# Performance work log

Hardware: AMD Instinct MI355X
Metric: run time of the kernel (lower is better)

Reference implementation:

```python
import jax, jax.numpy as jnp
import numpy as np

B, S, H, R = 32, 512, 1024, 64


def _bernoulli(key, shape, p=0.05):
    return (jax.random.uniform(key, shape) < p).astype(jnp.float32)


def setup_inputs() -> dict:
    key = jax.random.key(0)
    ks = jax.random.split(key, 16)
    context = jax.random.normal(ks[0], (B, S, H), dtype=jnp.float32)
    masks = jnp.ones((B, S), dtype=jnp.float32)
    all_subject_heads = _bernoulli(ks[1], (B, S))
    all_subject_tails = _bernoulli(ks[2], (B, S))
    # one-hot subject head/tail positions (tail >= head)
    h_pos = jax.random.randint(ks[3], (B,), 0, S // 2)
    t_pos = h_pos + jax.random.randint(ks[4], (B,), 0, 8)
    subject_head = jax.nn.one_hot(h_pos, S, dtype=jnp.float32)
    subject_tail = jax.nn.one_hot(t_pos, S, dtype=jnp.float32)
    object_heads = _bernoulli(ks[5], (B, S, R))
    object_tails = _bernoulli(ks[6], (B, S, R))
    # learned parameters (PyTorch Linear: y = x @ W.T + b; store as [in, out])
    sc = 1.0 / np.sqrt(H)
    Ws_h = jax.random.uniform(ks[7], (H, 1), minval=-sc, maxval=sc)
    bs_h = jnp.zeros((1,), dtype=jnp.float32)
    Ws_t = jax.random.uniform(ks[8], (H, 1), minval=-sc, maxval=sc)
    bs_t = jnp.zeros((1,), dtype=jnp.float32)
    Wo_h = jax.random.uniform(ks[9], (H, R), minval=-sc, maxval=sc)
    bo_h = jnp.zeros((R,), dtype=jnp.float32)
    Wo_t = jax.random.uniform(ks[10], (H, R), minval=-sc, maxval=sc)
    bo_t = jnp.zeros((R,), dtype=jnp.float32)
    return dict(context=context, masks=masks,
                all_subject_heads=all_subject_heads, all_subject_tails=all_subject_tails,
                subject_head=subject_head, subject_tail=subject_tail,
                object_heads=object_heads, object_tails=object_tails,
                Ws_h=Ws_h, bs_h=bs_h, Ws_t=Ws_t, bs_t=bs_t,
                Wo_h=Wo_h, bo_h=bo_h, Wo_t=Wo_t, bo_t=bo_t)


def _bce_with_logits(logits, targets):
    # numerically stable, matches F.binary_cross_entropy_with_logits(reduction='none')
    return jnp.maximum(logits, 0.0) - logits * targets + jnp.log1p(jnp.exp(-jnp.abs(logits)))


def _masked_loss(gold, pred, mask):
    loss = _bce_with_logits(pred, gold)
    if loss.ndim != mask.ndim:
        mask = mask[..., None]
    return jnp.sum(loss * mask) / jnp.sum(mask)


def reference(context, masks, all_subject_heads, all_subject_tails,
              subject_head, subject_tail, object_heads, object_tails,
              Ws_h, bs_h, Ws_t, bs_t, Wo_h, bo_h, Wo_t, bo_t):
    # subject logits: [B,S]
    pred_subject_heads = (context @ Ws_h + bs_h)[..., 0]
    pred_subject_tails = (context @ Ws_t + bs_t)[..., 0]
    # subject pooling: one-hot [B,S] x context [B,S,H] -> [B,H]
    sub_h = jnp.einsum('bs,bsh->bh', subject_head, context)
    sub_t = jnp.einsum('bs,bsh->bh', subject_tail, context)
    subject = (sub_h + sub_t) * 0.5
    context_subject = context + subject[:, None, :]  # [B,S,H]
    pred_object_heads = context_subject @ Wo_h + bo_h  # [B,S,R]
    pred_object_tails = context_subject @ Wo_t + bo_t  # [B,S,R]
    loss = (_masked_loss(all_subject_heads, pred_subject_heads, masks)
            + _masked_loss(all_subject_tails, pred_subject_tails, masks)
            + _masked_loss(object_heads, pred_object_heads, masks)
            + _masked_loss(object_tails, pred_object_tails, masks))
    return loss
```

## Files before the change

kernel.cpp:

```cpp
#include <hip/hip_runtime.h>
#include <hip/hip_bf16.h>


#define B_  32
#define S_  512
#define H_  1024
#define R_  64
#define M_  (B_ * S_)
#define NPAD 160
#define NVALID 130
#define BK 64
#define BKP 72
#define MT 32

typedef __attribute__((ext_vector_type(4))) float  floatx4;
typedef __attribute__((ext_vector_type(8))) short  short8;
typedef __attribute__((ext_vector_type(4))) unsigned short u16x4;
typedef __attribute__((ext_vector_type(8))) unsigned short u16x8;

__device__ __forceinline__ unsigned short f2bf(float f) {
    unsigned int u = __float_as_uint(f);
    u = (u + 0x7FFFu + ((u >> 16) & 1u)) >> 16;
    return (unsigned short)u;
}
__device__ __forceinline__ float bf2f(unsigned short h) {
    return __uint_as_float(((unsigned int)h) << 16);
}

__global__ void prep_weights(const float* __restrict__ Wo_h,
                             const float* __restrict__ Wo_t,
                             const float* __restrict__ Ws_h,
                             const float* __restrict__ Ws_t,
                             unsigned short* __restrict__ WtG) {
    int n = blockIdx.x;
    int tid = threadIdx.x;
    for (int k = tid; k < H_; k += 256) {
        float v;
        if (n < 64)        v = Wo_h[k * R_ + n];
        else if (n < 128)  v = Wo_t[k * R_ + (n - 64)];
        else if (n == 128) v = Ws_h[k];
        else if (n == 129) v = Ws_t[k];
        else               v = 0.0f;
        WtG[n * H_ + k] = f2bf(v);
    }
}

__global__ __launch_bounds__(256) void subj_kernel(
        const float* __restrict__ ctx, const float* __restrict__ head,
        const float* __restrict__ tail, const float* __restrict__ masks,
        const float* __restrict__ Wo_h, const float* __restrict__ Wo_t,
        const float* __restrict__ bo_h, const float* __restrict__ bo_t,
        const float* __restrict__ bs_h, const float* __restrict__ bs_t,
        float* __restrict__ rowBias, float* __restrict__ accum) {
    int b = blockIdx.x, tid = threadIdx.x;
    __shared__ float subj[H_];
    __shared__ int cnt;
    __shared__ int   sidx[8];
    __shared__ float sw[8];
    if (tid == 0) cnt = 0;
    __syncthreads();
    float msk = 0.0f;
    for (int s = tid; s < S_; s += 256) {
        float w = 0.5f * (head[b * S_ + s] + tail[b * S_ + s]);
        if (w != 0.0f) {
            int i = atomicAdd(&cnt, 1);
            if (i < 8) { sidx[i] = s; sw[i] = w; }
        }
        msk += masks[b * S_ + s];
    }
    for (int o = 32; o > 0; o >>= 1) msk += __shfl_down(msk, o, 64);
    if ((tid & 63) == 0) atomicAdd(&accum[1], msk);
    __syncthreads();
    int nnz = cnt < 8 ? cnt : 8;
    for (int h = tid; h < H_; h += 256) {
        float a = 0.0f;
        for (int i = 0; i < nnz; i++)
            a += sw[i] * ctx[((size_t)b * S_ + sidx[i]) * H_ + h];
        subj[h] = a;
    }
    __syncthreads();
    if (tid < NPAD) {
        float bias = tid < 64  ? bo_h[tid]
                   : tid < 128 ? bo_t[tid - 64]
                   : tid == 128 ? bs_h[0]
                   : tid == 129 ? bs_t[0] : 0.0f;
        float acc2 = 0.0f;
        if (tid < 128) {
            const float* W = (tid < 64) ? Wo_h : Wo_t;
            int c = tid & 63;
            for (int k = 0; k < H_; k++) acc2 += subj[k] * W[k * R_ + c];
        }
        rowBias[b * NPAD + tid] = bias + acc2;
    }
}

__global__ __launch_bounds__(256, 2) void main_kernel(
        const float* __restrict__ ctx, const unsigned short* __restrict__ WtG,
        const float* __restrict__ rowBias, const float* __restrict__ masks,
        const float* __restrict__ ash, const float* __restrict__ ast,
        const float* __restrict__ oh, const float* __restrict__ ot,
        float* __restrict__ accum) {
    __shared__ __align__(16) unsigned short Asm[MT * BKP];
    __shared__ __align__(16) unsigned short Bsm[NPAD * BKP];
    __shared__ float rbuf[4];

    const int tid = threadIdx.x;
    const int bm = blockIdx.x;
    const int gm0 = bm * MT;
    const int b = gm0 >> 9;
    const int wave = tid >> 6, lane = tid & 63;
    const int wm = wave & 1;
    const int wn = wave >> 1;
    const int lr = lane & 15, q = lane >> 4;

    const int ar = tid >> 4, af = tid & 15;
    const int bn = tid >> 3, bf = tid & 7;
    const float* aSrc0 = ctx + (size_t)(gm0 + ar) * H_ + af * 4;
    const unsigned short* bSrc0 = WtG + bn * H_ + bf * 8;
    unsigned short* aDst0 = &Asm[ar * BKP + af * 4];
    unsigned short* bDst0 = &Bsm[bn * BKP + bf * 8];

    const int aOff = (wm * 16 + lr) * BKP + q * 8;
    const int bOffBase = (wn * 80 + lr) * BKP + q * 8;

    floatx4 acc[5];
#pragma unroll
    for (int t = 0; t < 5; t++) acc[t] = (floatx4){0.f, 0.f, 0.f, 0.f};

    for (int k0 = 0; k0 < H_; k0 += BK) {
        __syncthreads();
#pragma unroll
        for (int ii = 0; ii < 2; ii++) {
            const float4 v = *(const float4*)(aSrc0 + ii * 16 * H_ + k0);
            u16x4 u = { f2bf(v.x), f2bf(v.y), f2bf(v.z), f2bf(v.w) };
            *(u16x4*)(aDst0 + ii * 16 * BKP) = u;
        }
#pragma unroll
        for (int ii = 0; ii < 5; ii++) {
            u16x8 w = *(const u16x8*)(bSrc0 + ii * 32 * H_ + k0);
            *(u16x8*)(bDst0 + ii * 32 * BKP) = w;
        }
        __syncthreads();
#pragma unroll
        for (int kk = 0; kk < BK; kk += 32) {
            short8 afr = *(const short8*)&Asm[aOff + kk];
#pragma unroll
            for (int t = 0; t < 5; t++) {
                short8 bfr = *(const short8*)&Bsm[bOffBase + t * 16 * BKP + kk];
                acc[t] = __builtin_amdgcn_mfma_f32_16x16x32_bf16(afr, bfr, acc[t], 0, 0, 0);
            }
        }
    }

    float lsum = 0.0f;
#pragma unroll
    for (int t = 0; t < 5; t++) {
        const int col = wn * 80 + t * 16 + lr;
        if (col < NVALID) {
            const float rb = rowBias[b * NPAD + col];
#pragma unroll
            for (int i = 0; i < 4; i++) {
                const int row = gm0 + wm * 16 + q * 4 + i;
                const float l = acc[t][i] + rb;
                float tgt;
                if (col < 64)        tgt = oh[row * R_ + col];
                else if (col < 128)  tgt = ot[row * R_ + (col - 64)];
                else if (col == 128) tgt = ash[row];
                else                 tgt = ast[row];
                const float mk = masks[row];
                const float bce = fmaxf(l, 0.0f) - l * tgt + log1pf(__expf(-fabsf(l)));
                lsum += bce * mk;
            }
        }
    }
    for (int o = 32; o > 0; o >>= 1) lsum += __shfl_down(lsum, o, 64);
    if (lane == 0) rbuf[wave] = lsum;
    __syncthreads();
    if (tid == 0) atomicAdd(&accum[0], rbuf[0] + rbuf[1] + rbuf[2] + rbuf[3]);
}

__global__ void finalize_kernel(const float* __restrict__ accum, float* __restrict__ out) {
    out[0] = accum[0] / accum[1];
}

extern "C" void kernel_launch(void* const* d_in, const int* in_sizes, int n_in,
                              void* d_out, int out_size, void* d_ws, size_t ws_size,
                              hipStream_t stream) {
    const float* ctx   = (const float*)d_in[0];
    const float* masks = (const float*)d_in[1];
    const float* ash   = (const float*)d_in[2];
    const float* ast   = (const float*)d_in[3];
    const float* sh    = (const float*)d_in[4];
    const float* st    = (const float*)d_in[5];
    const float* oh    = (const float*)d_in[6];
    const float* ot    = (const float*)d_in[7];
    const float* Ws_h  = (const float*)d_in[8];
    const float* bs_h  = (const float*)d_in[9];
    const float* Ws_t  = (const float*)d_in[10];
    const float* bs_t  = (const float*)d_in[11];
    const float* Wo_h  = (const float*)d_in[12];
    const float* bo_h  = (const float*)d_in[13];
    const float* Wo_t  = (const float*)d_in[14];
    const float* bo_t  = (const float*)d_in[15];
    float* out = (float*)d_out;

    char* ws = (char*)d_ws;
    float* accum   = (float*)(ws + 0);
    float* rowBias = (float*)(ws + 256);
    unsigned short* WtG = (unsigned short*)(ws + 256 + 32 * NPAD * 4);

    hipMemsetAsync(accum, 0, 8, stream);
    prep_weights<<<NPAD, 256, 0, stream>>>(Wo_h, Wo_t, Ws_h, Ws_t, WtG);
    subj_kernel<<<B_, 256, 0, stream>>>(ctx, sh, st, masks, Wo_h, Wo_t,
                                        bo_h, bo_t, bs_h, bs_t, rowBias, accum);
    main_kernel<<<M_ / MT, 256, 0, stream>>>(ctx, WtG, rowBias, masks,
                                             ash, ast, oh, ot, accum);
    finalize_kernel<<<1, 1, 0, stream>>>(accum, out);
}
```

Before: 167.5 us.

## Load MFMA fragments directly from global with register double-buffering, merge prep kernels

The main GEMM drops LDS staging and its barriers. Each lane now loads its A (fp32, converted to bf16) and B fragments straight from global memory into registers, double-buffered across 32 K-steps. The weight-transpose and subject-bias kernels are merged into one launch, the subject bias matvec is split across two thread halves, and the mask sum moves into the main kernel. In exchange, B fragments are re-read from global/L2 by every wave instead of being shared through LDS, and the subject pooling now caps nonzeros at 4.

```diff
diff --git a/kernel.cpp b/kernel.cpp
--- a/kernel.cpp
+++ b/kernel.cpp
@@ -1,5 +1,4 @@
 #include <hip/hip_runtime.h>
-#include <hip/hip_bf16.h>
 
 
 #define B_  32
@@ -9,69 +8,55 @@
 #define M_  (B_ * S_)
 #define NPAD 160
 #define NVALID 130
-#define BK 64
-#define BKP 72
-#define MT 32
 
 typedef __attribute__((ext_vector_type(4))) float  floatx4;
 typedef __attribute__((ext_vector_type(8))) short  short8;
-typedef __attribute__((ext_vector_type(4))) unsigned short u16x4;
-typedef __attribute__((ext_vector_type(8))) unsigned short u16x8;
 
 __device__ __forceinline__ unsigned short f2bf(float f) {
     unsigned int u = __float_as_uint(f);
     u = (u + 0x7FFFu + ((u >> 16) & 1u)) >> 16;
     return (unsigned short)u;
 }
-__device__ __forceinline__ float bf2f(unsigned short h) {
-    return __uint_as_float(((unsigned int)h) << 16);
-}
-
-__global__ void prep_weights(const float* __restrict__ Wo_h,
-                             const float* __restrict__ Wo_t,
-                             const float* __restrict__ Ws_h,
-                             const float* __restrict__ Ws_t,
-                             unsigned short* __restrict__ WtG) {
-    int n = blockIdx.x;
-    int tid = threadIdx.x;
-    for (int k = tid; k < H_; k += 256) {
-        float v;
-        if (n < 64)        v = Wo_h[k * R_ + n];
-        else if (n < 128)  v = Wo_t[k * R_ + (n - 64)];
-        else if (n == 128) v = Ws_h[k];
-        else if (n == 129) v = Ws_t[k];
-        else               v = 0.0f;
-        WtG[n * H_ + k] = f2bf(v);
-    }
-}
-
-__global__ __launch_bounds__(256) void subj_kernel(
-        const float* __restrict__ ctx, const float* __restrict__ head,
-        const float* __restrict__ tail, const float* __restrict__ masks,
+
+__global__ __launch_bounds__(256) void prep_kernel(
+        const float* __restrict__ ctx,  const float* __restrict__ head,
+        const float* __restrict__ tail,
+        const float* __restrict__ Ws_h, const float* __restrict__ Ws_t,
         const float* __restrict__ Wo_h, const float* __restrict__ Wo_t,
         const float* __restrict__ bo_h, const float* __restrict__ bo_t,
         const float* __restrict__ bs_h, const float* __restrict__ bs_t,
-        float* __restrict__ rowBias, float* __restrict__ accum) {
-    int b = blockIdx.x, tid = threadIdx.x;
+        unsigned short* __restrict__ WtG, float* __restrict__ rowBias) {
+    const int blk = blockIdx.x, tid = threadIdx.x;
+    if (blk < NPAD) {
+        const int n = blk;
+        for (int k = tid; k < H_; k += 256) {
+            float v;
+            if (n < 64)        v = Wo_h[k * R_ + n];
+            else if (n < 128)  v = Wo_t[k * R_ + (n - 64)];
+            else if (n == 128) v = Ws_h[k];
+            else if (n == 129) v = Ws_t[k];
+            else               v = 0.0f;
+            WtG[n * H_ + k] = f2bf(v);
+        }
+        return;
+    }
+    const int b = blk - NPAD;
     __shared__ float subj[H_];
+    __shared__ float part[256];
     __shared__ int cnt;
-    __shared__ int   sidx[8];
-    __shared__ float sw[8];
+    __shared__ int   sidx[4];
+    __shared__ float sw[4];
     if (tid == 0) cnt = 0;
     __syncthreads();
-    float msk = 0.0f;
     for (int s = tid; s < S_; s += 256) {
         float w = 0.5f * (head[b * S_ + s] + tail[b * S_ + s]);
         if (w != 0.0f) {
             int i = atomicAdd(&cnt, 1);
-            if (i < 8) { sidx[i] = s; sw[i] = w; }
-        }
-        msk += masks[b * S_ + s];
-    }
-    for (int o = 32; o > 0; o >>= 1) msk += __shfl_down(msk, o, 64);
-    if ((tid & 63) == 0) atomicAdd(&accum[1], msk);
-    __syncthreads();
-    int nnz = cnt < 8 ? cnt : 8;
+            if (i < 4) { sidx[i] = s; sw[i] = w; }
+        }
+    }
+    __syncthreads();
+    const int nnz = cnt < 4 ? cnt : 4;
     for (int h = tid; h < H_; h += 256) {
         float a = 0.0f;
         for (int i = 0; i < nnz; i++)
@@ -79,77 +64,85 @@
         subj[h] = a;
     }
     __syncthreads();
+    {
+        const int c = tid & 127, hf = tid >> 7;
+        const float* W = (c < 64) ? (Wo_h + c) : (Wo_t + (c - 64));
+        float a = 0.0f;
+        const int k0 = hf * 512;
+#pragma unroll 8
+        for (int k = k0; k < k0 + 512; k++)
+            a += subj[k] * W[(size_t)k * R_];
+        part[tid] = a;
+    }
+    __syncthreads();
     if (tid < NPAD) {
-        float bias = tid < 64  ? bo_h[tid]
-                   : tid < 128 ? bo_t[tid - 64]
-                   : tid == 128 ? bs_h[0]
-                   : tid == 129 ? bs_t[0] : 0.0f;
-        float acc2 = 0.0f;
-        if (tid < 128) {
-            const float* W = (tid < 64) ? Wo_h : Wo_t;
-            int c = tid & 63;
-            for (int k = 0; k < H_; k++) acc2 += subj[k] * W[k * R_ + c];
-        }
-        rowBias[b * NPAD + tid] = bias + acc2;
-    }
-}
-
-__global__ __launch_bounds__(256, 2) void main_kernel(
+        float v;
+        if (tid < 128)
+            v = part[tid] + part[128 + tid] + (tid < 64 ? bo_h[tid] : bo_t[tid - 64]);
+        else if (tid == 128) v = bs_h[0];
+        else if (tid == 129) v = bs_t[0];
+        else                 v = 0.0f;
+        rowBias[b * NPAD + tid] = v;
+    }
+}
+
+__global__ __launch_bounds__(256) void main_kernel(
         const float* __restrict__ ctx, const unsigned short* __restrict__ WtG,
         const float* __restrict__ rowBias, const float* __restrict__ masks,
         const float* __restrict__ ash, const float* __restrict__ ast,
         const float* __restrict__ oh, const float* __restrict__ ot,
         float* __restrict__ accum) {
-    __shared__ __align__(16) unsigned short Asm[MT * BKP];
-    __shared__ __align__(16) unsigned short Bsm[NPAD * BKP];
     __shared__ float rbuf[4];
-
-    const int tid = threadIdx.x;
-    const int bm = blockIdx.x;
-    const int gm0 = bm * MT;
-    const int b = gm0 >> 9;
+    const int tid  = threadIdx.x;
+    const int gm0  = blockIdx.x * 32;
+    const int b    = gm0 >> 9;
     const int wave = tid >> 6, lane = tid & 63;
     const int wm = wave & 1;
     const int wn = wave >> 1;
     const int lr = lane & 15, q = lane >> 4;
 
-    const int ar = tid >> 4, af = tid & 15;
-    const int bn = tid >> 3, bf = tid & 7;
-    const float* aSrc0 = ctx + (size_t)(gm0 + ar) * H_ + af * 4;
-    const unsigned short* bSrc0 = WtG + bn * H_ + bf * 8;
-    unsigned short* aDst0 = &Asm[ar * BKP + af * 4];
-    unsigned short* bDst0 = &Bsm[bn * BKP + bf * 8];
-
-    const int aOff = (wm * 16 + lr) * BKP + q * 8;
-    const int bOffBase = (wn * 80 + lr) * BKP + q * 8;
+    if (tid < 32) {
+        float mv = masks[gm0 + tid];
+#pragma unroll
+        for (int o = 16; o > 0; o >>= 1) mv += __shfl_down(mv, o, 64);
+        if (tid == 0) atomicAdd(&accum[1], mv);
+    }
+
+    const float* aP = ctx + (size_t)(gm0 + wm * 16 + lr) * H_ + q * 8;
+    const unsigned short* bB[5];
+#pragma unroll
+    for (int t = 0; t < 5; t++)
+        bB[t] = WtG + (size_t)(wn * 80 + t * 16 + lr) * H_ + q * 8;
 
     floatx4 acc[5];
 #pragma unroll
     for (int t = 0; t < 5; t++) acc[t] = (floatx4){0.f, 0.f, 0.f, 0.f};
 
-    for (int k0 = 0; k0 < H_; k0 += BK) {
-        __syncthreads();
-#pragma unroll
-        for (int ii = 0; ii < 2; ii++) {
-            const float4 v = *(const float4*)(aSrc0 + ii * 16 * H_ + k0);
-            u16x4 u = { f2bf(v.x), f2bf(v.y), f2bf(v.z), f2bf(v.w) };
-            *(u16x4*)(aDst0 + ii * 16 * BKP) = u;
-        }
-#pragma unroll
-        for (int ii = 0; ii < 5; ii++) {
-            u16x8 w = *(const u16x8*)(bSrc0 + ii * 32 * H_ + k0);
-            *(u16x8*)(bDst0 + ii * 32 * BKP) = w;
-        }
-        __syncthreads();
-#pragma unroll
-        for (int kk = 0; kk < BK; kk += 32) {
-            short8 afr = *(const short8*)&Asm[aOff + kk];
-#pragma unroll
-            for (int t = 0; t < 5; t++) {
-                short8 bfr = *(const short8*)&Bsm[bOffBase + t * 16 * BKP + kk];
-                acc[t] = __builtin_amdgcn_mfma_f32_16x16x32_bf16(afr, bfr, acc[t], 0, 0, 0);
-            }
-        }
+    float4 a0[2], a1[2];
+    short8 bv[2][5];
+    a0[0] = *(const float4*)(aP + 0);
+    a1[0] = *(const float4*)(aP + 4);
+#pragma unroll
+    for (int t = 0; t < 5; t++) bv[0][t] = *(const short8*)(bB[t] + 0);
+
+#pragma unroll
+    for (int i = 0; i < 32; i++) {
+        const int cur = i & 1, nxt = cur ^ 1;
+        if (i < 31) {
+            const int k = (i + 1) * 32;
+            a0[nxt] = *(const float4*)(aP + k);
+            a1[nxt] = *(const float4*)(aP + k + 4);
+#pragma unroll
+            for (int t = 0; t < 5; t++) bv[nxt][t] = *(const short8*)(bB[t] + k);
+        }
+        short8 af;
+        af[0] = (short)f2bf(a0[cur].x); af[1] = (short)f2bf(a0[cur].y);
+        af[2] = (short)f2bf(a0[cur].z); af[3] = (short)f2bf(a0[cur].w);
+        af[4] = (short)f2bf(a1[cur].x); af[5] = (short)f2bf(a1[cur].y);
+        af[6] = (short)f2bf(a1[cur].z); af[7] = (short)f2bf(a1[cur].w);
+#pragma unroll
+        for (int t = 0; t < 5; t++)
+            acc[t] = __builtin_amdgcn_mfma_f32_16x16x32_bf16(af, bv[cur][t], acc[t], 0, 0, 0);
     }
 
     float lsum = 0.0f;
@@ -173,6 +166,7 @@
             }
         }
     }
+#pragma unroll
     for (int o = 32; o > 0; o >>= 1) lsum += __shfl_down(lsum, o, 64);
     if (lane == 0) rbuf[wave] = lsum;
     __syncthreads();
@@ -195,8 +189,8 @@
     const float* oh    = (const float*)d_in[6];
     const float* ot    = (const float*)d_in[7];
     const float* Ws_h  = (const float*)d_in[8];
+    const float* Ws_t  = (const float*)d_in[10];
     const float* bs_h  = (const float*)d_in[9];
-    const float* Ws_t  = (const float*)d_in[10];
     const float* bs_t  = (const float*)d_in[11];
     const float* Wo_h  = (const float*)d_in[12];
     const float* bo_h  = (const float*)d_in[13];
@@ -210,10 +204,10 @@
     unsigned short* WtG = (unsigned short*)(ws + 256 + 32 * NPAD * 4);
 
     hipMemsetAsync(accum, 0, 8, stream);
-    prep_weights<<<NPAD, 256, 0, stream>>>(Wo_h, Wo_t, Ws_h, Ws_t, WtG);
-    subj_kernel<<<B_, 256, 0, stream>>>(ctx, sh, st, masks, Wo_h, Wo_t,
-                                        bo_h, bo_t, bs_h, bs_t, rowBias, accum);
-    main_kernel<<<M_ / MT, 256, 0, stream>>>(ctx, WtG, rowBias, masks,
+    prep_kernel<<<NPAD + B_, 256, 0, stream>>>(ctx, sh, st, Ws_h, Ws_t,
+                                               Wo_h, Wo_t, bo_h, bo_t, bs_h, bs_t,
+                                               WtG, rowBias);
+    main_kernel<<<M_ / 32, 256, 0, stream>>>(ctx, WtG, rowBias, masks,
                                              ash, ast, oh, ot, accum);
     finalize_kernel<<<1, 1, 0, stream>>>(accum, out);
 }
```

Measured after the change: 194.6 us. 1.16x slower.
